# Performance work log

Hardware: AMD Instinct MI355X
Metric: run time of the kernel (lower is better)

The kernel has to match this reference:

```python
import jax, jax.numpy as jnp
import numpy as np

BLOCK = 64      # InformationEntropyAnalyzer block_size
BINS = 256      # InformationEntropyAnalyzer num_bins
EPS = 1e-12


def setup_inputs() -> dict:
    key = jax.random.key(0)
    x = jax.random.normal(key, (8, 64, 256, 256), dtype=jnp.float32)
    return {"x": x}


def _block_entropy(blocks):
    """Shannon entropy per block, matching np.histogram(density=True) math.

    blocks: (B, n) float32. Returns (B,) float32.
    """
    B, n = blocks.shape
    bmin = jnp.min(blocks, axis=1, keepdims=True)            # (B,1)
    bmax = jnp.max(blocks, axis=1, keepdims=True)            # (B,1)
    width = (bmax - bmin) / BINS                              # uniform bin width
    width_safe = jnp.where(width > 0, width, 1.0)
    # np.histogram: rightmost edge inclusive -> floor + clip reproduces it
    idx = jnp.clip(jnp.floor((blocks - bmin) / width_safe), 0, BINS - 1).astype(jnp.int32)
    row = jnp.arange(B, dtype=jnp.int32)[:, None]
    flat = (row * BINS + idx).reshape(-1)
    counts = jax.ops.segment_sum(
        jnp.ones((B * n,), jnp.float32), flat, num_segments=B * BINS
    ).reshape(B, BINS)
    density = counts / (n * width_safe)                       # density=True normalization
    p = density + EPS
    p = p / jnp.sum(p, axis=1, keepdims=True)
    return -jnp.sum(p * jnp.log2(p), axis=1)


def reference(x):
    """Faithful JAX version of InformationEntropyAnalyzer._compute_4d_entropy.

    Per (n,c) slice: split HxW into BLOCKxBLOCK tiles, compute Shannon entropy
    of the 256-bin histogram of each tile, then bilinearly upsample
    (align_corners=False, i.e. half-pixel, = jax.image.resize 'linear')
    back to (H, W).  Output: (N, C, H, W) entropy map.
    """
    N, C, H, W = x.shape
    nbh, nbw = H // BLOCK, W // BLOCK  # evenly divisible by construction
    blocks = (
        x.reshape(N, C, nbh, BLOCK, nbw, BLOCK)
        .transpose(0, 1, 2, 4, 3, 5)
        .reshape(N * C * nbh * nbw, BLOCK * BLOCK)
    )
    ent = _block_entropy(blocks).reshape(N, C, nbh, nbw)
    # F.interpolate(mode='bilinear', align_corners=False) == half-pixel linear resize
    return jax.image.resize(ent, (N, C, H, W), method='linear')
```

## Files before the change

### kernel.cpp

```cpp
#include <hip/hip_runtime.h>

#define NBINS 256
#define EPSF 1e-12f

typedef float v4f __attribute__((ext_vector_type(4)));

__global__ __launch_bounds__(256, 2) void fused_kernel(const float* __restrict__ x,
                                                       float* __restrict__ out) {
    const int nc   = blockIdx.x;
    const int t    = threadIdx.x;
    const int lane = t & 63;
    const int wave = t >> 6;

    __shared__ unsigned int hist[4][NBINS];
    __shared__ float ent_s[16];

    const float* cbase = x + ((size_t)nc << 16) + (size_t)wave * 64;
    unsigned int* h = hist[wave];

    v4f va[16], vb[16];

#define ISSUE(buf, s)                                                             \
    _Pragma("unroll")                                                             \
    for (int k = 0; k < 16; ++k) {                                                \
        const int f = lane + (k << 6);                    \
        buf[k] = *reinterpret_cast<const v4f*>(                                   \
            cbase + (size_t)(s) * (64 * 256) + (size_t)(f >> 4) * 256 + (f & 15) * 4); \
    }

#define PROCESS(buf, s)                                                           \
    {                                                                             \
        float lmin = INFINITY, lmax = -INFINITY;                                  \
        _Pragma("unroll")                                                         \
        for (int k = 0; k < 16; ++k) {                                            \
            lmin = fminf(lmin, fminf(fminf(buf[k].x, buf[k].y),                   \
                                     fminf(buf[k].z, buf[k].w)));                 \
            lmax = fmaxf(lmax, fmaxf(fmaxf(buf[k].x, buf[k].y),                   \
                                     fmaxf(buf[k].z, buf[k].w)));                 \
        }                                                                         \
        _Pragma("unroll")                                                         \
        for (int off = 32; off > 0; off >>= 1) {                                  \
            lmin = fminf(lmin, __shfl_xor(lmin, off));                            \
            lmax = fmaxf(lmax, __shfl_xor(lmax, off));                            \
        }                                                                         \
        uint4 z; z.x = z.y = z.z = z.w = 0u;       \
        reinterpret_cast<uint4*>(h)[lane] = z;                                    \
        const float width = (lmax - lmin) * (1.0f / NBINS);                       \
        const float wsafe = (width > 0.0f) ? width : 1.0f;                        \
        const float inv   = 1.0f / wsafe;                                         \
        const float coff  = -lmin * inv;                                          \
        _Pragma("unroll")                                                         \
        for (int k = 0; k < 16; ++k) {                                            \
            float vals[4] = {buf[k].x, buf[k].y, buf[k].z, buf[k].w};             \
            _Pragma("unroll")                                                     \
            for (int j = 0; j < 4; ++j) {                                         \
                      \
                int bin = (int)fmaf(vals[j], inv, coff);                          \
                bin = min(bin, 255);                                              \
                atomicAdd(&h[bin], 1u);                                           \
            }                                                                     \
        }                                                                         \
        const uint4 c    = reinterpret_cast<const uint4*>(h)[lane];               \
        const float pden = inv * (1.0f / 4096.0f);            \
        const float p0 = (float)c.x * pden + EPSF;                                \
        const float p1 = (float)c.y * pden + EPSF;                                \
        const float p2 = (float)c.z * pden + EPSF;                                \
        const float p3 = (float)c.w * pden + EPSF;                                \
        float s_ = p0 + p1 + p2 + p3;                                             \
        _Pragma("unroll")                                                         \
        for (int off = 32; off > 0; off >>= 1) s_ += __shfl_xor(s_, off);         \
        const float itot = 1.0f / s_;                                             \
        const float q0 = p0 * itot, q1 = p1 * itot;                               \
        const float q2 = p2 * itot, q3 = p3 * itot;                               \
        float e = q0 * log2f(q0) + q1 * log2f(q1)                                 \
                + q2 * log2f(q2) + q3 * log2f(q3);                                \
        _Pragma("unroll")                                                         \
        for (int off = 32; off > 0; off >>= 1) e += __shfl_xor(e, off);           \
        if (lane == 0) ent_s[((s) << 2) + wave] = -e;                             \
    }

    const int x4 = lane;
    const int ix = (int)floorf(((x4 << 2) + 0.5f) * 0.015625f - 0.5f);
    const int x0 = max(ix, 0), x1 = min(ix + 1, 3);
    v4f wv[4];
#pragma unroll
    for (int j = 0; j < 4; ++j) {
        const float fx = ((x4 << 2) + j + 0.5f) * 0.015625f - 0.5f;
        const float wx = fx - floorf(fx);
        const float a  = 1.0f - wx, bb = wx;
        wv[j].x = ((x0 == 0) ? a : 0.0f) + ((x1 == 0) ? bb : 0.0f);
        wv[j].y = ((x0 == 1) ? a : 0.0f) + ((x1 == 1) ? bb : 0.0f);
        wv[j].z = ((x0 == 2) ? a : 0.0f) + ((x1 == 2) ? bb : 0.0f);
        wv[j].w = ((x0 == 3) ? a : 0.0f) + ((x1 == 3) ? bb : 0.0f);
    }
    const v4f* er = reinterpret_cast<const v4f*>(ent_s);
    v4f* out4 = reinterpret_cast<v4f*>(out) + ((size_t)nc << 14);

#define WQ(q)                                                                     \
    _Pragma("unroll")                                                             \
    for (int i = 0; i < 16; ++i) {                                                \
        const int   y   = ((q) << 6) + (wave << 4) + i;                           \
        const float fy  = (y + 0.5f) * 0.015625f - 0.5f;                          \
        const float fiy = floorf(fy);                                             \
        const float wy  = fy - fiy;                                               \
        const int   iy  = (int)fiy;                                               \
        const int   y0  = max(iy, 0), y1 = min(iy + 1, 3);                        \
        const v4f r0 = er[y0];                 \
        const v4f r1 = er[y1];                                                    \
        v4f rv = r0 * (1.0f - wy) + r1 * wy;                                      \
        v4f o;                                                                    \
        o.x = rv.x * wv[0].x + rv.y * wv[0].y + rv.z * wv[0].z + rv.w * wv[0].w;  \
        o.y = rv.x * wv[1].x + rv.y * wv[1].y + rv.z * wv[1].z + rv.w * wv[1].w;  \
        o.z = rv.x * wv[2].x + rv.y * wv[2].y + rv.z * wv[2].z + rv.w * wv[2].w;  \
        o.w = rv.x * wv[3].x + rv.y * wv[3].y + rv.z * wv[3].z + rv.w * wv[3].w;  \
        out4[(y << 6) + x4] = o;                                                  \
    }

    ISSUE(va, 0)
    ISSUE(vb, 1)
    PROCESS(va, 0)
    ISSUE(va, 2)
    PROCESS(vb, 1)
    ISSUE(vb, 3)
    __syncthreads();
    WQ(0)
    PROCESS(va, 2)
    __syncthreads();
    WQ(1)
    PROCESS(vb, 3)
    __syncthreads();
    WQ(2)
    WQ(3)

#undef ISSUE
#undef PROCESS
#undef WQ
}

extern "C" void kernel_launch(void* const* d_in, const int* in_sizes, int n_in,
                              void* d_out, int out_size, void* d_ws, size_t ws_size,
                              hipStream_t stream) {
    const float* x   = (const float*)d_in[0];
    float*       out = (float*)d_out;
    fused_kernel<<<512, 256, 0, stream>>>(x, out);
}
```

Measured before the change: 43.44 us.

## Specialize waves into histogram producers and output writers with LDS flag sync

Doubles the block to 512 threads. Four waves compute block entropies and signal completion via shared-memory counters, while four extra waves spin-wait on those flags and write the upsampled output rows. This overlaps output stores with histogram computation and replaces block-wide barriers. The launch bound of 512 threads with 4 blocks per CU constrains registers heavily, which risks spilling the 32 v4f load buffers, and the spin-waits burn issue slots.

```diff
diff --git a/kernel.cpp b/kernel.cpp
--- a/kernel.cpp
+++ b/kernel.cpp
@@ -5,7 +5,7 @@
 
 typedef float v4f __attribute__((ext_vector_type(4)));
 
-__global__ __launch_bounds__(256, 2) void fused_kernel(const float* __restrict__ x,
+__global__ __launch_bounds__(512, 4) void fused_kernel(const float* __restrict__ x,
                                                        float* __restrict__ out) {
     const int nc   = blockIdx.x;
     const int t    = threadIdx.x;
@@ -14,11 +14,58 @@
 
     __shared__ unsigned int hist[4][NBINS];
     __shared__ float ent_s[16];
+    __shared__ unsigned int ent_ready[4];
 
-    const float* cbase = x + ((size_t)nc << 16) + (size_t)wave * 64;
-    unsigned int* h = hist[wave];
+    if (t < 4) ent_ready[t] = 0u;
+    __syncthreads();
 
-    v4f va[16], vb[16];
+    const int x4 = lane;
+    const int ix = (int)floorf(((x4 << 2) + 0.5f) * 0.015625f - 0.5f);
+    const int x0 = max(ix, 0), x1 = min(ix + 1, 3);
+    v4f wv[4];
+#pragma unroll
+    for (int j = 0; j < 4; ++j) {
+        const float fx = ((x4 << 2) + j + 0.5f) * 0.015625f - 0.5f;
+        const float wx = fx - floorf(fx);
+        const float a  = 1.0f - wx, bb = wx;
+        wv[j].x = ((x0 == 0) ? a : 0.0f) + ((x1 == 0) ? bb : 0.0f);
+        wv[j].y = ((x0 == 1) ? a : 0.0f) + ((x1 == 1) ? bb : 0.0f);
+        wv[j].z = ((x0 == 2) ? a : 0.0f) + ((x1 == 2) ? bb : 0.0f);
+        wv[j].w = ((x0 == 3) ? a : 0.0f) + ((x1 == 3) ? bb : 0.0f);
+    }
+    const v4f* er = reinterpret_cast<const v4f*>(ent_s);
+    v4f* out4 = reinterpret_cast<v4f*>(out) + ((size_t)nc << 14);
+
+#define WROWS(ystart, nrows)                                                      \
+    _Pragma("unroll")                                                             \
+    for (int i = 0; i < (nrows); ++i) {                                           \
+        const int   y   = (ystart) + i;                                           \
+        const float fy  = (y + 0.5f) * 0.015625f - 0.5f;                          \
+        const float fiy = floorf(fy);                                             \
+        const float wy  = fy - fiy;                                               \
+        const int   iy  = (int)fiy;                                               \
+        const int   y0  = max(iy, 0), y1 = min(iy + 1, 3);                        \
+        const v4f r0 = er[y0];                 \
+        const v4f r1 = er[y1];                                                    \
+        v4f rv = r0 * (1.0f - wy) + r1 * wy;                                      \
+        v4f o;                                                                    \
+        o.x = rv.x * wv[0].x + rv.y * wv[0].y + rv.z * wv[0].z + rv.w * wv[0].w;  \
+        o.y = rv.x * wv[1].x + rv.y * wv[1].y + rv.z * wv[1].z + rv.w * wv[1].w;  \
+        o.z = rv.x * wv[2].x + rv.y * wv[2].y + rv.z * wv[2].z + rv.w * wv[2].w;  \
+        o.w = rv.x * wv[3].x + rv.y * wv[3].y + rv.z * wv[3].z + rv.w * wv[3].w;  \
+        out4[(y << 6) + lane] = o;                                                \
+    }
+
+#define WAITROW(s)                                                                \
+    do {                                                                          \
+        while (((volatile unsigned int*)ent_ready)[s] < 4u) {}                    \
+        asm volatile("" ::: "memory");                                            \
+    } while (0)
+
+    if (wave < 4) {
+        const float* cbase = x + ((size_t)nc << 16) + (size_t)wave * 64;
+        unsigned int* h = hist[wave];
+        v4f va[16], vb[16];
 
 #define ISSUE(buf, s)                                                             \
     _Pragma("unroll")                                                             \
@@ -76,65 +123,39 @@
                 + q2 * log2f(q2) + q3 * log2f(q3);                                \
         _Pragma("unroll")                                                         \
         for (int off = 32; off > 0; off >>= 1) e += __shfl_xor(e, off);           \
-        if (lane == 0) ent_s[((s) << 2) + wave] = -e;                             \
+        if (lane == 0) {                                                          \
+            ent_s[((s) << 2) + wave] = -e;                                        \
+            __threadfence_block();                   \
+            atomicAdd(&ent_ready[s], 1u);                                         \
+        }                                                                         \
     }
 
-    const int x4 = lane;
-    const int ix = (int)floorf(((x4 << 2) + 0.5f) * 0.015625f - 0.5f);
-    const int x0 = max(ix, 0), x1 = min(ix + 1, 3);
-    v4f wv[4];
-#pragma unroll
-    for (int j = 0; j < 4; ++j) {
-        const float fx = ((x4 << 2) + j + 0.5f) * 0.015625f - 0.5f;
-        const float wx = fx - floorf(fx);
-        const float a  = 1.0f - wx, bb = wx;
-        wv[j].x = ((x0 == 0) ? a : 0.0f) + ((x1 == 0) ? bb : 0.0f);
-        wv[j].y = ((x0 == 1) ? a : 0.0f) + ((x1 == 1) ? bb : 0.0f);
-        wv[j].z = ((x0 == 2) ? a : 0.0f) + ((x1 == 2) ? bb : 0.0f);
-        wv[j].w = ((x0 == 3) ? a : 0.0f) + ((x1 == 3) ? bb : 0.0f);
-    }
-    const v4f* er = reinterpret_cast<const v4f*>(ent_s);
-    v4f* out4 = reinterpret_cast<v4f*>(out) + ((size_t)nc << 14);
-
-#define WQ(q)                                                                     \
-    _Pragma("unroll")                                                             \
-    for (int i = 0; i < 16; ++i) {                                                \
-        const int   y   = ((q) << 6) + (wave << 4) + i;                           \
-        const float fy  = (y + 0.5f) * 0.015625f - 0.5f;                          \
-        const float fiy = floorf(fy);                                             \
-        const float wy  = fy - fiy;                                               \
-        const int   iy  = (int)fiy;                                               \
-        const int   y0  = max(iy, 0), y1 = min(iy + 1, 3);                        \
-        const v4f r0 = er[y0];                 \
-        const v4f r1 = er[y1];                                                    \
-        v4f rv = r0 * (1.0f - wy) + r1 * wy;                                      \
-        v4f o;                                                                    \
-        o.x = rv.x * wv[0].x + rv.y * wv[0].y + rv.z * wv[0].z + rv.w * wv[0].w;  \
-        o.y = rv.x * wv[1].x + rv.y * wv[1].y + rv.z * wv[1].z + rv.w * wv[1].w;  \
-        o.z = rv.x * wv[2].x + rv.y * wv[2].y + rv.z * wv[2].z + rv.w * wv[2].w;  \
-        o.w = rv.x * wv[3].x + rv.y * wv[3].y + rv.z * wv[3].z + rv.w * wv[3].w;  \
-        out4[(y << 6) + x4] = o;                                                  \
-    }
-
-    ISSUE(va, 0)
-    ISSUE(vb, 1)
-    PROCESS(va, 0)
-    ISSUE(va, 2)
-    PROCESS(vb, 1)
-    ISSUE(vb, 3)
-    __syncthreads();
-    WQ(0)
-    PROCESS(va, 2)
-    __syncthreads();
-    WQ(1)
-    PROCESS(vb, 3)
-    __syncthreads();
-    WQ(2)
-    WQ(3)
-
+        ISSUE(va, 0)
+        ISSUE(vb, 1)
+        PROCESS(va, 0)
+        ISSUE(va, 2)
+        PROCESS(vb, 1)
+        ISSUE(vb, 3)
+        PROCESS(va, 2)
+        PROCESS(vb, 3)
 #undef ISSUE
 #undef PROCESS
-#undef WQ
+
+        WAITROW(2);
+        WAITROW(3);
+        WROWS(208 + wave * 12, 12)
+    } else {
+        const int w = wave - 4;
+        WAITROW(0);
+        WAITROW(1);
+        WROWS(w * 24, 24)
+        WAITROW(2);
+        WROWS(96 + w * 16, 16)
+        WAITROW(3);
+        WROWS(160 + w * 12, 12)
+    }
+#undef WROWS
+#undef WAITROW
 }
 
 extern "C" void kernel_launch(void* const* d_in, const int* in_sizes, int n_in,
@@ -142,5 +163,5 @@
                               hipStream_t stream) {
     const float* x   = (const float*)d_in[0];
     float*       out = (float*)d_out;
-    fused_kernel<<<512, 256, 0, stream>>>(x, out);
+    fused_kernel<<<512, 512, 0, stream>>>(x, out);
 }
```

Result: slower. 101.2 us (+133.0%).
